# Kernel tuning notes

Hardware: AMD Instinct MI355X
Metric: run time of the kernel (lower is better)

## Reference

```python
import jax, jax.numpy as jnp
import numpy as np

B, T, D_IN, H, D_OUT = 256, 2048, 128, 128, 128


def setup_inputs() -> dict:
    key = jax.random.key(0)
    ks = jax.random.split(key, 7)
    s_in = 1.0 / np.sqrt(H)
    return {
        "x": jax.random.normal(ks[0], (B, T, D_IN), dtype=jnp.float32),
        "Wih": jax.random.normal(ks[1], (4 * H, D_IN), dtype=jnp.float32) * s_in,
        "Whh": jax.random.normal(ks[2], (4 * H, H), dtype=jnp.float32) * s_in,
        "bih": jax.random.normal(ks[3], (4 * H,), dtype=jnp.float32) * s_in,
        "bhh": jax.random.normal(ks[4], (4 * H,), dtype=jnp.float32) * s_in,
        "Wo": jax.random.normal(ks[5], (D_OUT, H), dtype=jnp.float32) * s_in,
        "bo": jax.random.normal(ks[6], (D_OUT,), dtype=jnp.float32) * s_in,
    }


def reference(x, Wih, Whh, bih, bhh, Wo, bo):
    # LSTM recurrence over time; module returns only the last step's
    # output projection (outputs[:, -1, :]).
    batch, seq_len, _ = x.shape
    h0 = jnp.zeros((batch, Whh.shape[1]), dtype=x.dtype)
    c0 = jnp.zeros_like(h0)
    # Precompute input-side gate projections for all timesteps in one GEMM.
    xg = jnp.einsum('btd,gd->btg', x, Wih) + bih + bhh  # [B, T, 4H]
    xg = jnp.swapaxes(xg, 0, 1)  # [T, B, 4H] for scan

    def step(carry, xg_t):
        h, c = carry
        gates = xg_t + h @ Whh.T  # [B, 4H]
        i, f, g, o = jnp.split(gates, 4, axis=-1)
        i = jax.nn.sigmoid(i)
        f = jax.nn.sigmoid(f)
        g = jnp.tanh(g)
        o = jax.nn.sigmoid(o)
        c = f * c + i * g
        h = o * jnp.tanh(c)
        return (h, c), None

    (h_last, _), _ = jax.lax.scan(step, (h0, c0), xg)
    return h_last @ Wo.T + bo  # [B, D_OUT]
```

## Files before the change

kernel.cpp:

```cpp
#include <hip/hip_runtime.h>
#include <hip/hip_fp16.h>

#define B_  256
#define T_  2048
#define D_  128
#define H_  128
#define CH  32
#define NCH (T_ / CH)
#define XGP (4 * H_ + 8)

#define NLOG2E  (-1.4426950408889634f)
#define LOG2E2  ( 2.8853900817779268f)

typedef __attribute__((ext_vector_type(8))) _Float16 half8v;
typedef __attribute__((ext_vector_type(4))) float    floatx4;

static __device__ __forceinline__ unsigned pkh(float a, float b) {
  return __builtin_bit_cast(unsigned, __builtin_amdgcn_cvt_pkrtz(a, b));
}
static __device__ __forceinline__ float h2f_lo(unsigned u) {
  return __half2float(__ushort_as_half((unsigned short)(u & 0xffffu)));
}
static __device__ __forceinline__ float h2f_hi(unsigned u) {
  return __half2float(__ushort_as_half((unsigned short)(u >> 16)));
}
#define SEL4(v, n) (((n) & 2) ? (((n) & 1) ? (v)[3] : (v)[2]) \
                              : (((n) & 1) ? (v)[1] : (v)[0]))

__global__ __attribute__((amdgpu_flat_work_group_size(512, 512),
                          amdgpu_waves_per_eu(2, 2)))
void lstm_mfma3(
    const float* __restrict__ x,   const float* __restrict__ Wih,
    const float* __restrict__ Whh, const float* __restrict__ bih,
    const float* __restrict__ bhh, const float* __restrict__ Wo,
    const float* __restrict__ bo,  float* __restrict__ out)
{
  __shared__ unsigned       xs[CH][68];
  __shared__ unsigned short xgf[CH][XGP];
  __shared__ __align__(16) unsigned hbuf[2][64];

  const int tid  = threadIdx.x;
  const int b    = blockIdx.x;
  const int lane = tid & 63;
  const int wv   = tid >> 6;
  const int quad = lane >> 4;
  const int m16  = lane & 15;

  uint4 wa[4][4];
  #pragma unroll
  for (int mt = 0; mt < 4; ++mt) {
    float s = (mt == 2) ? LOG2E2 : NLOG2E;
    const float4* p = (const float4*)(Whh + (size_t)(mt * 128 + wv * 16 + m16) * H_);
    #pragma unroll
    for (int kf = 0; kf < 4; ++kf) {
      float4 f0 = p[kf * 8 + quad * 2];
      float4 f1 = p[kf * 8 + quad * 2 + 1];
      uint4 u;
      u.x = pkh(f0.x * s, f0.y * s);  u.y = pkh(f0.z * s, f0.w * s);
      u.z = pkh(f1.x * s, f1.y * s);  u.w = pkh(f1.z * s, f1.w * s);
      wa[mt][kf] = u;
    }
  }

  const float sW = ((wv >> 1) == 2) ? LOG2E2 : NLOG2E;
  uint4 wb[4][4];
  float bv[4];
  #pragma unroll
  for (int nt = 0; nt < 4; ++nt) {
    int gcol = wv * 64 + nt * 16 + m16;
    const float4* p = (const float4*)(Wih + (size_t)gcol * D_);
    #pragma unroll
    for (int kf = 0; kf < 4; ++kf) {
      float4 f0 = p[kf * 8 + quad * 2];
      float4 f1 = p[kf * 8 + quad * 2 + 1];
      uint4 u;
      u.x = pkh(f0.x * sW, f0.y * sW);  u.y = pkh(f0.z * sW, f0.w * sW);
      u.z = pkh(f1.x * sW, f1.y * sW);  u.w = pkh(f1.z * sW, f1.w * sW);
      wb[nt][kf] = u;
    }
    bv[nt] = (bih[gcol] + bhh[gcol]) * sW;
  }

  if (tid < 128) hbuf[tid >> 6][tid & 63] = 0u;
  uint4 hfr[4] = {{0,0,0,0},{0,0,0,0},{0,0,0,0},{0,0,0,0}};
  floatx4 zf = {0.f, 0.f, 0.f, 0.f};
  float c = 0.0f;
  __syncthreads();

  const float* xb = x + (size_t)b * T_ * D_;

  for (int ch = 0; ch < NCH; ++ch) {
    const float4* xsrc = (const float4*)(xb + (size_t)ch * CH * D_);
    #pragma unroll
    for (int i = 0; i < 2; ++i) {
      int fi = i * 512 + tid;
      float4 v = xsrc[fi];
      int t  = fi >> 5;
      int kp = (fi & 31) * 2;
      xs[t][kp]     = pkh(v.x, v.y);
      xs[t][kp + 1] = pkh(v.z, v.w);
    }
    __syncthreads();

    #pragma unroll
    for (int mt = 0; mt < 2; ++mt) {
      half8v af[4];
      #pragma unroll
      for (int kf = 0; kf < 4; ++kf)
        af[kf] = __builtin_bit_cast(half8v,
                   *(const uint4*)&xs[mt * 16 + m16][kf * 16 + quad * 4]);
      #pragma unroll
      for (int nt = 0; nt < 4; ++nt) {
        floatx4 acc = zf;
        #pragma unroll
        for (int kf = 0; kf < 4; ++kf)
          acc = __builtin_amdgcn_mfma_f32_16x16x32_f16(
              af[kf], __builtin_bit_cast(half8v, wb[nt][kf]), acc, 0, 0, 0);
        int gcol = wv * 64 + nt * 16 + m16;
        int jc   = gcol & 127, gt = gcol >> 7;
        #pragma unroll
        for (int r = 0; r < 4; ++r) {
          int trow = mt * 16 + quad * 4 + r;
          xgf[trow][jc * 4 + gt] =
              __half_as_ushort(__float2half(acc[r] + bv[nt]));
        }
      }
    }
    __syncthreads();

    #pragma unroll 2
    for (int tt = 0; tt < CH; ++tt) {
      const int rp = tt & 1;
      unsigned long long xv = 0ull;
      if (m16 < 4) {
        xv = *(const unsigned long long*)&xgf[tt][(wv * 16 + quad * 4 + m16) * 4];
        #pragma unroll
        for (int kf = 0; kf < 4; ++kf)
          hfr[kf] = *(const uint4*)&hbuf[rp][kf * 16 + quad * 4];
      }
      floatx4 a0, a1, a2, a3;
      {
        half8v hb = __builtin_bit_cast(half8v, hfr[0]);
        a0 = __builtin_amdgcn_mfma_f32_16x16x32_f16(
                 __builtin_bit_cast(half8v, wa[0][0]), hb, zf, 0, 0, 0);
        a1 = __builtin_amdgcn_mfma_f32_16x16x32_f16(
                 __builtin_bit_cast(half8v, wa[1][0]), hb, zf, 0, 0, 0);
        a2 = __builtin_amdgcn_mfma_f32_16x16x32_f16(
                 __builtin_bit_cast(half8v, wa[2][0]), hb, zf, 0, 0, 0);
        a3 = __builtin_amdgcn_mfma_f32_16x16x32_f16(
                 __builtin_bit_cast(half8v, wa[3][0]), hb, zf, 0, 0, 0);
      }
      #pragma unroll
      for (int kf = 1; kf < 4; ++kf) {
        half8v hb = __builtin_bit_cast(half8v, hfr[kf]);
        a0 = __builtin_amdgcn_mfma_f32_16x16x32_f16(
                 __builtin_bit_cast(half8v, wa[0][kf]), hb, a0, 0, 0, 0);
        a1 = __builtin_amdgcn_mfma_f32_16x16x32_f16(
                 __builtin_bit_cast(half8v, wa[1][kf]), hb, a1, 0, 0, 0);
        a2 = __builtin_amdgcn_mfma_f32_16x16x32_f16(
                 __builtin_bit_cast(half8v, wa[2][kf]), hb, a2, 0, 0, 0);
        a3 = __builtin_amdgcn_mfma_f32_16x16x32_f16(
                 __builtin_bit_cast(half8v, wa[3][kf]), hb, a3, 0, 0, 0);
      }
      if (m16 < 4) {
        const int n  = m16;
        const int jl = wv * 16 + quad * 4 + n;
        unsigned xlo = (unsigned)xv, xhi = (unsigned)(xv >> 32);
        float pi = SEL4(a0, n) + h2f_lo(xlo);
        float pf = SEL4(a1, n) + h2f_hi(xlo);
        float pg = SEL4(a2, n) + h2f_lo(xhi);
        float po = SEL4(a3, n) + h2f_hi(xhi);
        float gi = __builtin_amdgcn_rcpf(1.0f + __builtin_amdgcn_exp2f(pi));
        float gf = __builtin_amdgcn_rcpf(1.0f + __builtin_amdgcn_exp2f(pf));
        float go = __builtin_amdgcn_rcpf(1.0f + __builtin_amdgcn_exp2f(po));
        float gg = 1.0f - 2.0f * __builtin_amdgcn_rcpf(1.0f + __builtin_amdgcn_exp2f(pg));
        c = gf * c + gi * gg;
        float tc = 1.0f - 2.0f * __builtin_amdgcn_rcpf(
                       1.0f + __builtin_amdgcn_exp2f(c * LOG2E2));
        float h = go * tc;
        ((unsigned short*)hbuf[rp ^ 1])[jl] = __half_as_ushort(__float2half(h));
      }
      __syncthreads();
    }
  }

  if (tid < H_) {
    float acc = bo[tid];
    const float4* wr = (const float4*)(Wo + (size_t)tid * H_);
    const uint2* hp = (const uint2*)hbuf[0];
    #pragma unroll
    for (int k4 = 0; k4 < 32; ++k4) {
      float4 w  = wr[k4];
      uint2  hu = hp[k4];
      acc += w.x * h2f_lo(hu.x) + w.y * h2f_hi(hu.x)
           + w.z * h2f_lo(hu.y) + w.w * h2f_hi(hu.y);
    }
    out[(size_t)b * H_ + tid] = acc;
  }
}

extern "C" void kernel_launch(void* const* d_in, const int* in_sizes, int n_in,
                              void* d_out, int out_size, void* d_ws, size_t ws_size,
                              hipStream_t stream) {
  (void)in_sizes; (void)n_in; (void)d_ws; (void)ws_size; (void)out_size;
  const float* x   = (const float*)d_in[0];
  const float* Wih = (const float*)d_in[1];
  const float* Whh = (const float*)d_in[2];
  const float* bih = (const float*)d_in[3];
  const float* bhh = (const float*)d_in[4];
  const float* Wo  = (const float*)d_in[5];
  const float* bo  = (const float*)d_in[6];
  lstm_mfma3<<<B_, 512, 0, stream>>>(x, Wih, Whh, bih, bhh, Wo, bo, (float*)d_out);
}
```

Baseline: 1.280 ms.

## Replace per-step recurrent MFMA matvec with packed fdot2 and DPP reductions

The recurrent h·Whh product, a single-row matvec per block, previously ran as 16 MFMAs per wave, and most of the output was wasted. It now uses v_dot2 half-precision dot products. Each group of 4 lanes splits the K dimension, and partial sums are combined with DPP row shifts. The precomputed input gates are pre-scaled by 0.25 so that the bias, added in every one of the four partial lanes, sums back correctly. This shortens the serial per-step latency and lets all lanes do gate math, at the cost of more VALU instructions and 64 weight registers.

```diff
diff --git a/kernel.cpp b/kernel.cpp
--- a/kernel.cpp
+++ b/kernel.cpp
@@ -13,6 +13,7 @@
 #define LOG2E2  ( 2.8853900817779268f)
 
 typedef __attribute__((ext_vector_type(8))) _Float16 half8v;
+typedef __attribute__((ext_vector_type(2))) _Float16 half2v;
 typedef __attribute__((ext_vector_type(4))) float    floatx4;
 
 static __device__ __forceinline__ unsigned pkh(float a, float b) {
@@ -24,12 +25,20 @@
 static __device__ __forceinline__ float h2f_hi(unsigned u) {
   return __half2float(__ushort_as_half((unsigned short)(u >> 16)));
 }
-#define SEL4(v, n) (((n) & 2) ? (((n) & 1) ? (v)[3] : (v)[2]) \
-                              : (((n) & 1) ? (v)[1] : (v)[0]))
+static __device__ __forceinline__ float fdot2(unsigned h, unsigned w, float c) {
+  return __builtin_amdgcn_fdot2(__builtin_bit_cast(half2v, h),
+                                __builtin_bit_cast(half2v, w), c, false);
+}
+template <int CTRL>
+static __device__ __forceinline__ float dppadd(float v) {
+  int t = __builtin_amdgcn_update_dpp(0, __builtin_bit_cast(int, v),
+                                      CTRL, 0xF, 0xF, false);
+  return v + __builtin_bit_cast(float, t);
+}
 
 __global__ __attribute__((amdgpu_flat_work_group_size(512, 512),
                           amdgpu_waves_per_eu(2, 2)))
-void lstm_mfma3(
+void lstm_dot2(
     const float* __restrict__ x,   const float* __restrict__ Wih,
     const float* __restrict__ Whh, const float* __restrict__ bih,
     const float* __restrict__ bhh, const float* __restrict__ Wo,
@@ -45,20 +54,21 @@
   const int wv   = tid >> 6;
   const int quad = lane >> 4;
   const int m16  = lane & 15;
-
-  uint4 wa[4][4];
+  const int unit_l = quad * 4 + (m16 & 3);
+  const int unit_g = wv * 16 + unit_l;
+  const int kq   = m16 >> 2;
+
+  unsigned wd[4][16];
   #pragma unroll
-  for (int mt = 0; mt < 4; ++mt) {
-    float s = (mt == 2) ? LOG2E2 : NLOG2E;
-    const float4* p = (const float4*)(Whh + (size_t)(mt * 128 + wv * 16 + m16) * H_);
-    #pragma unroll
-    for (int kf = 0; kf < 4; ++kf) {
-      float4 f0 = p[kf * 8 + quad * 2];
-      float4 f1 = p[kf * 8 + quad * 2 + 1];
-      uint4 u;
-      u.x = pkh(f0.x * s, f0.y * s);  u.y = pkh(f0.z * s, f0.w * s);
-      u.z = pkh(f1.x * s, f1.y * s);  u.w = pkh(f1.z * s, f1.w * s);
-      wa[mt][kf] = u;
+  for (int g = 0; g < 4; ++g) {
+    float s = (g == 2) ? LOG2E2 : NLOG2E;
+    const float4* p =
+        (const float4*)(Whh + (size_t)(g * 128 + unit_g) * H_) + kq * 8;
+    #pragma unroll
+    for (int q = 0; q < 8; ++q) {
+      float4 f = p[q];
+      wd[g][q * 2]     = pkh(f.x * s, f.y * s);
+      wd[g][q * 2 + 1] = pkh(f.z * s, f.w * s);
     }
   }
 
@@ -82,8 +92,7 @@
   }
 
   if (tid < 128) hbuf[tid >> 6][tid & 63] = 0u;
-  uint4 hfr[4] = {{0,0,0,0},{0,0,0,0},{0,0,0,0},{0,0,0,0}};
-  floatx4 zf = {0.f, 0.f, 0.f, 0.f};
+  const floatx4 zf = {0.f, 0.f, 0.f, 0.f};
   float c = 0.0f;
   __syncthreads();
 
@@ -122,7 +131,7 @@
         for (int r = 0; r < 4; ++r) {
           int trow = mt * 16 + quad * 4 + r;
           xgf[trow][jc * 4 + gt] =
-              __half_as_ushort(__float2half(acc[r] + bv[nt]));
+              __half_as_ushort(__float2half((acc[r] + bv[nt]) * 0.25f));
         }
       }
     }
@@ -131,55 +140,40 @@
     #pragma unroll 2
     for (int tt = 0; tt < CH; ++tt) {
       const int rp = tt & 1;
-      unsigned long long xv = 0ull;
-      if (m16 < 4) {
-        xv = *(const unsigned long long*)&xgf[tt][(wv * 16 + quad * 4 + m16) * 4];
-        #pragma unroll
-        for (int kf = 0; kf < 4; ++kf)
-          hfr[kf] = *(const uint4*)&hbuf[rp][kf * 16 + quad * 4];
+      unsigned long long xv =
+          *(const unsigned long long*)&xgf[tt][unit_g * 4];
+      const unsigned* hb = &hbuf[rp][kq * 16];
+      unsigned hs[16];
+      *(uint4*)&hs[0]  = *(const uint4*)(hb + 0);
+      *(uint4*)&hs[4]  = *(const uint4*)(hb + 4);
+      *(uint4*)&hs[8]  = *(const uint4*)(hb + 8);
+      *(uint4*)&hs[12] = *(const uint4*)(hb + 12);
+      unsigned xlo = (unsigned)xv, xhi = (unsigned)(xv >> 32);
+      float ai = h2f_lo(xlo), af_ = h2f_hi(xlo);
+      float ag = h2f_lo(xhi), ao  = h2f_hi(xhi);
+      #pragma unroll
+      for (int p = 0; p < 16; ++p) {
+        ai  = fdot2(hs[p], wd[0][p], ai);
+        af_ = fdot2(hs[p], wd[1][p], af_);
+        ag  = fdot2(hs[p], wd[2][p], ag);
+        ao  = fdot2(hs[p], wd[3][p], ao);
       }
-      floatx4 a0, a1, a2, a3;
-      {
-        half8v hb = __builtin_bit_cast(half8v, hfr[0]);
-        a0 = __builtin_amdgcn_mfma_f32_16x16x32_f16(
-                 __builtin_bit_cast(half8v, wa[0][0]), hb, zf, 0, 0, 0);
-        a1 = __builtin_amdgcn_mfma_f32_16x16x32_f16(
-                 __builtin_bit_cast(half8v, wa[1][0]), hb, zf, 0, 0, 0);
-        a2 = __builtin_amdgcn_mfma_f32_16x16x32_f16(
-                 __builtin_bit_cast(half8v, wa[2][0]), hb, zf, 0, 0, 0);
-        a3 = __builtin_amdgcn_mfma_f32_16x16x32_f16(
-                 __builtin_bit_cast(half8v, wa[3][0]), hb, zf, 0, 0, 0);
-      }
-      #pragma unroll
-      for (int kf = 1; kf < 4; ++kf) {
-        half8v hb = __builtin_bit_cast(half8v, hfr[kf]);
-        a0 = __builtin_amdgcn_mfma_f32_16x16x32_f16(
-                 __builtin_bit_cast(half8v, wa[0][kf]), hb, a0, 0, 0, 0);
-        a1 = __builtin_amdgcn_mfma_f32_16x16x32_f16(
-                 __builtin_bit_cast(half8v, wa[1][kf]), hb, a1, 0, 0, 0);
-        a2 = __builtin_amdgcn_mfma_f32_16x16x32_f16(
-                 __builtin_bit_cast(half8v, wa[2][kf]), hb, a2, 0, 0, 0);
-        a3 = __builtin_amdgcn_mfma_f32_16x16x32_f16(
-                 __builtin_bit_cast(half8v, wa[3][kf]), hb, a3, 0, 0, 0);
-      }
-      if (m16 < 4) {
-        const int n  = m16;
-        const int jl = wv * 16 + quad * 4 + n;
-        unsigned xlo = (unsigned)xv, xhi = (unsigned)(xv >> 32);
-        float pi = SEL4(a0, n) + h2f_lo(xlo);
-        float pf = SEL4(a1, n) + h2f_hi(xlo);
-        float pg = SEL4(a2, n) + h2f_lo(xhi);
-        float po = SEL4(a3, n) + h2f_hi(xhi);
-        float gi = __builtin_amdgcn_rcpf(1.0f + __builtin_amdgcn_exp2f(pi));
-        float gf = __builtin_amdgcn_rcpf(1.0f + __builtin_amdgcn_exp2f(pf));
-        float go = __builtin_amdgcn_rcpf(1.0f + __builtin_amdgcn_exp2f(po));
-        float gg = 1.0f - 2.0f * __builtin_amdgcn_rcpf(1.0f + __builtin_amdgcn_exp2f(pg));
-        c = gf * c + gi * gg;
-        float tc = 1.0f - 2.0f * __builtin_amdgcn_rcpf(
-                       1.0f + __builtin_amdgcn_exp2f(c * LOG2E2));
-        float h = go * tc;
-        ((unsigned short*)hbuf[rp ^ 1])[jl] = __half_as_ushort(__float2half(h));
-      }
+      ai  = dppadd<0x124>(dppadd<0x128>(ai));
+      af_ = dppadd<0x124>(dppadd<0x128>(af_));
+      ag  = dppadd<0x124>(dppadd<0x128>(ag));
+      ao  = dppadd<0x124>(dppadd<0x128>(ao));
+      float gi = __builtin_amdgcn_rcpf(1.0f + __builtin_amdgcn_exp2f(ai));
+      float gf = __builtin_amdgcn_rcpf(1.0f + __builtin_amdgcn_exp2f(af_));
+      float go = __builtin_amdgcn_rcpf(1.0f + __builtin_amdgcn_exp2f(ao));
+      float gg = 1.0f - 2.0f * __builtin_amdgcn_rcpf(
+                     1.0f + __builtin_amdgcn_exp2f(ag));
+      c = gf * c + gi * gg;
+      float tc = 1.0f - 2.0f * __builtin_amdgcn_rcpf(
+                     1.0f + __builtin_amdgcn_exp2f(c * LOG2E2));
+      float h = go * tc;
+      if (m16 < 4)
+        ((unsigned short*)hbuf[rp ^ 1])[unit_g] =
+            __half_as_ushort(__float2half(h));
       __syncthreads();
     }
   }
@@ -210,5 +204,5 @@
   const float* bhh = (const float*)d_in[4];
   const float* Wo  = (const float*)d_in[5];
   const float* bo  = (const float*)d_in[6];
-  lstm_mfma3<<<B_, 512, 0, stream>>>(x, Wih, Whh, bih, bhh, Wo, bo, (float*)d_out);
-}
+  lstm_dot2<<<B_, 512, 0, stream>>>(x, Wih, Whh, bih, bhh, Wo, bo, (float*)d_out);
+}
```

Measured after the change: 1.413 ms. 10.4% more time.

## Spread LSTM gate nonlinearities across 16 lanes with cross-lane swizzle exchange

Applied to the files above, without the earlier changes.

In the old code, only 4 of every 16 lanes computed all four gate activations for one hidden unit. Now all 16 lanes each compute one gate activation, and the i*g product, f and o are exchanged through ds_swizzle and DPP. The input-projection buffer is transposed to a [gate-column][time] layout, so each lane loads four timesteps of its own gate in one 64-bit read, and packed half writes replace scalar stores. This shortens the serial per-step transcendental chain on the critical path, at the cost of extra cross-lane ops and more complex lane-selection logic.

```diff
diff --git a/kernel.cpp b/kernel.cpp
--- a/kernel.cpp
+++ b/kernel.cpp
@@ -7,7 +7,7 @@
 #define H_  128
 #define CH  32
 #define NCH (T_ / CH)
-#define XGP (4 * H_ + 8)
+#define XTP 36
 
 #define NLOG2E  (-1.4426950408889634f)
 #define LOG2E2  ( 2.8853900817779268f)
@@ -29,14 +29,14 @@
 
 __global__ __attribute__((amdgpu_flat_work_group_size(512, 512),
                           amdgpu_waves_per_eu(2, 2)))
-void lstm_mfma3(
+void lstm_dense(
     const float* __restrict__ x,   const float* __restrict__ Wih,
     const float* __restrict__ Whh, const float* __restrict__ bih,
     const float* __restrict__ bhh, const float* __restrict__ Wo,
     const float* __restrict__ bo,  float* __restrict__ out)
 {
   __shared__ unsigned       xs[CH][68];
-  __shared__ unsigned short xgf[CH][XGP];
+  __shared__ __align__(16) unsigned short xgT[4 * H_][XTP];
   __shared__ __align__(16) unsigned hbuf[2][64];
 
   const int tid  = threadIdx.x;
@@ -45,6 +45,8 @@
   const int wv   = tid >> 6;
   const int quad = lane >> 4;
   const int m16  = lane & 15;
+  const int rsel = m16 & 3;
+  const int gsel = m16 >> 2;
 
   uint4 wa[4][4];
   #pragma unroll
@@ -82,12 +84,12 @@
   }
 
   if (tid < 128) hbuf[tid >> 6][tid & 63] = 0u;
-  uint4 hfr[4] = {{0,0,0,0},{0,0,0,0},{0,0,0,0},{0,0,0,0}};
-  floatx4 zf = {0.f, 0.f, 0.f, 0.f};
+  const floatx4 zf = {0.f, 0.f, 0.f, 0.f};
   float c = 0.0f;
   __syncthreads();
 
   const float* xb = x + (size_t)b * T_ * D_;
+  const int mycol = ((wv * 16 + quad * 4 + rsel) << 2) | gsel;
 
   for (int ch = 0; ch < NCH; ++ch) {
     const float4* xsrc = (const float4*)(xb + (size_t)ch * CH * D_);
@@ -117,70 +119,84 @@
           acc = __builtin_amdgcn_mfma_f32_16x16x32_f16(
               af[kf], __builtin_bit_cast(half8v, wb[nt][kf]), acc, 0, 0, 0);
         int gcol = wv * 64 + nt * 16 + m16;
-        int jc   = gcol & 127, gt = gcol >> 7;
-        #pragma unroll
-        for (int r = 0; r < 4; ++r) {
-          int trow = mt * 16 + quad * 4 + r;
-          xgf[trow][jc * 4 + gt] =
-              __half_as_ushort(__float2half(acc[r] + bv[nt]));
-        }
+        int cu   = ((gcol & 127) << 2) | (gcol >> 7);
+        uint2 pk;
+        pk.x = pkh(acc[0] + bv[nt], acc[1] + bv[nt]);
+        pk.y = pkh(acc[2] + bv[nt], acc[3] + bv[nt]);
+        *(unsigned long long*)&xgT[cu][mt * 16 + quad * 4] =
+            __builtin_bit_cast(unsigned long long, pk);
       }
     }
     __syncthreads();
 
-    #pragma unroll 2
-    for (int tt = 0; tt < CH; ++tt) {
-      const int rp = tt & 1;
-      unsigned long long xv = 0ull;
-      if (m16 < 4) {
-        xv = *(const unsigned long long*)&xgf[tt][(wv * 16 + quad * 4 + m16) * 4];
+    for (int tt4 = 0; tt4 < CH; tt4 += 4) {
+      unsigned long long xq4 =
+          *(const unsigned long long*)&xgT[mycol][tt4];
+      #pragma unroll
+      for (int tq = 0; tq < 4; ++tq) {
+        const int tt = tt4 + tq;
+        const int rp = tt & 1;
+        uint4 hfr[4];
         #pragma unroll
         for (int kf = 0; kf < 4; ++kf)
           hfr[kf] = *(const uint4*)&hbuf[rp][kf * 16 + quad * 4];
-      }
-      floatx4 a0, a1, a2, a3;
-      {
-        half8v hb = __builtin_bit_cast(half8v, hfr[0]);
-        a0 = __builtin_amdgcn_mfma_f32_16x16x32_f16(
-                 __builtin_bit_cast(half8v, wa[0][0]), hb, zf, 0, 0, 0);
-        a1 = __builtin_amdgcn_mfma_f32_16x16x32_f16(
-                 __builtin_bit_cast(half8v, wa[1][0]), hb, zf, 0, 0, 0);
-        a2 = __builtin_amdgcn_mfma_f32_16x16x32_f16(
-                 __builtin_bit_cast(half8v, wa[2][0]), hb, zf, 0, 0, 0);
-        a3 = __builtin_amdgcn_mfma_f32_16x16x32_f16(
-                 __builtin_bit_cast(half8v, wa[3][0]), hb, zf, 0, 0, 0);
-      }
-      #pragma unroll
-      for (int kf = 1; kf < 4; ++kf) {
-        half8v hb = __builtin_bit_cast(half8v, hfr[kf]);
-        a0 = __builtin_amdgcn_mfma_f32_16x16x32_f16(
-                 __builtin_bit_cast(half8v, wa[0][kf]), hb, a0, 0, 0, 0);
-        a1 = __builtin_amdgcn_mfma_f32_16x16x32_f16(
-                 __builtin_bit_cast(half8v, wa[1][kf]), hb, a1, 0, 0, 0);
-        a2 = __builtin_amdgcn_mfma_f32_16x16x32_f16(
-                 __builtin_bit_cast(half8v, wa[2][kf]), hb, a2, 0, 0, 0);
-        a3 = __builtin_amdgcn_mfma_f32_16x16x32_f16(
-                 __builtin_bit_cast(half8v, wa[3][kf]), hb, a3, 0, 0, 0);
-      }
-      if (m16 < 4) {
-        const int n  = m16;
-        const int jl = wv * 16 + quad * 4 + n;
-        unsigned xlo = (unsigned)xv, xhi = (unsigned)(xv >> 32);
-        float pi = SEL4(a0, n) + h2f_lo(xlo);
-        float pf = SEL4(a1, n) + h2f_hi(xlo);
-        float pg = SEL4(a2, n) + h2f_lo(xhi);
-        float po = SEL4(a3, n) + h2f_hi(xhi);
-        float gi = __builtin_amdgcn_rcpf(1.0f + __builtin_amdgcn_exp2f(pi));
-        float gf = __builtin_amdgcn_rcpf(1.0f + __builtin_amdgcn_exp2f(pf));
-        float go = __builtin_amdgcn_rcpf(1.0f + __builtin_amdgcn_exp2f(po));
-        float gg = 1.0f - 2.0f * __builtin_amdgcn_rcpf(1.0f + __builtin_amdgcn_exp2f(pg));
-        c = gf * c + gi * gg;
+
+        floatx4 a0, a1, a2, a3;
+        {
+          half8v hb = __builtin_bit_cast(half8v, hfr[0]);
+          a0 = __builtin_amdgcn_mfma_f32_16x16x32_f16(
+                   __builtin_bit_cast(half8v, wa[0][0]), hb, zf, 0, 0, 0);
+          a1 = __builtin_amdgcn_mfma_f32_16x16x32_f16(
+                   __builtin_bit_cast(half8v, wa[1][0]), hb, zf, 0, 0, 0);
+          a2 = __builtin_amdgcn_mfma_f32_16x16x32_f16(
+                   __builtin_bit_cast(half8v, wa[2][0]), hb, zf, 0, 0, 0);
+          a3 = __builtin_amdgcn_mfma_f32_16x16x32_f16(
+                   __builtin_bit_cast(half8v, wa[3][0]), hb, zf, 0, 0, 0);
+        }
+        #pragma unroll
+        for (int kf = 1; kf < 4; ++kf) {
+          half8v hb = __builtin_bit_cast(half8v, hfr[kf]);
+          a0 = __builtin_amdgcn_mfma_f32_16x16x32_f16(
+                   __builtin_bit_cast(half8v, wa[0][kf]), hb, a0, 0, 0, 0);
+          a1 = __builtin_amdgcn_mfma_f32_16x16x32_f16(
+                   __builtin_bit_cast(half8v, wa[1][kf]), hb, a1, 0, 0, 0);
+          a2 = __builtin_amdgcn_mfma_f32_16x16x32_f16(
+                   __builtin_bit_cast(half8v, wa[2][kf]), hb, a2, 0, 0, 0);
+          a3 = __builtin_amdgcn_mfma_f32_16x16x32_f16(
+                   __builtin_bit_cast(half8v, wa[3][kf]), hb, a3, 0, 0, 0);
+        }
+
+        float s0 = SEL4(a0, rsel), s1 = SEL4(a1, rsel);
+        float s2 = SEL4(a2, rsel), s3 = SEL4(a3, rsel);
+        float sg = SEL4(((floatx4){s0, s1, s2, s3}), gsel);
+        float xh = __half2float(__ushort_as_half(
+                       (unsigned short)(xq4 >> (16 * tq))));
+        float pre = sg + xh;
+        float rr  = __builtin_amdgcn_rcpf(1.0f + __builtin_amdgcn_exp2f(pre));
+        float val = (gsel == 2) ? fmaf(-2.0f, rr, 1.0f) : rr;
+
+        int vb = __builtin_bit_cast(int, val);
+        int r1 = __builtin_amdgcn_ds_swizzle(vb, 0x101F);
+        int r2 = __builtin_amdgcn_update_dpp(0, vb, 0x128, 0xF, 0xF, false);
+        int r3 = __builtin_amdgcn_ds_swizzle(r2, 0x101F);
+        float R1 = __builtin_bit_cast(float, r1);
+        float R2 = __builtin_bit_cast(float, r2);
+        float R3 = __builtin_bit_cast(float, r3);
+
+        const bool b0 = (gsel & 1) != 0, b1 = (gsel & 2) != 0;
+        float P  = b0 ? R1 * R3 : val * R2;
+        float gf = b0 ? (b1 ? R2 : val) : (b1 ? R3 : R1);
+        float go = b0 ? (b1 ? val : R2) : (b1 ? R1 : R3);
+
+        c = fmaf(gf, c, P);
         float tc = 1.0f - 2.0f * __builtin_amdgcn_rcpf(
                        1.0f + __builtin_amdgcn_exp2f(c * LOG2E2));
         float h = go * tc;
-        ((unsigned short*)hbuf[rp ^ 1])[jl] = __half_as_ushort(__float2half(h));
+        if (gsel == 0)
+          ((unsigned short*)hbuf[rp ^ 1])[wv * 16 + quad * 4 + rsel] =
+              __half_as_ushort(__float2half(h));
+        __syncthreads();
       }
-      __syncthreads();
     }
   }
 
@@ -210,5 +226,5 @@
   const float* bhh = (const float*)d_in[4];
   const float* Wo  = (const float*)d_in[5];
   const float* bo  = (const float*)d_in[6];
-  lstm_mfma3<<<B_, 512, 0, stream>>>(x, Wih, Whh, bih, bhh, Wo, bo, (float*)d_out);
-}
+  lstm_dense<<<B_, 512, 0, stream>>>(x, Wih, Whh, bih, bhh, Wo, bo, (float*)d_out);
+}
```

Result: slower. 1.355 ms (+5.9%).
